# Performance work log

Hardware: AMD Instinct MI355X
Metric: run time of the kernel (lower is better)

Reference implementation:

```python
import jax, jax.numpy as jnp
import numpy as np

TEMP = 0.5
ALPHA, BETA, GAMMA, LAMB = 1e-3, 5e-4, 1e-3, 5e-6
IMG = 1024.0  # img_metas img_shape (H_img, W_img)
LN_EPS = 1e-5


def setup_inputs() -> dict:
    key = jax.random.key(0)
    ks = jax.random.split(key, 20)
    N, C, H, W, NB = 8, 256, 128, 128, 20
    preds_S = jax.random.normal(ks[0], (N, C, H, W), jnp.float32)
    preds_T = jax.random.normal(ks[1], (N, C, H, W), jnp.float32)
    # valid boxes (tl_x, tl_y, br_x, br_y) in pixel coords within [0, IMG]
    raw = jax.random.uniform(ks[2], (N, NB, 4), jnp.float32)
    x1 = raw[..., 0] * 0.7 * IMG
    y1 = raw[..., 1] * 0.7 * IMG
    x2 = jnp.minimum(x1 + (0.05 + raw[..., 2] * 0.25) * IMG, IMG)
    y2 = jnp.minimum(y1 + (0.05 + raw[..., 3] * 0.25) * IMG, IMG)
    gt_bboxes = jnp.stack([x1, y1, x2, y2], axis=-1)
    s = 1.0 / np.sqrt(C)
    s2 = 1.0 / np.sqrt(C // 2)
    mk = lambda k, shape, sc: jax.random.normal(k, shape, jnp.float32) * sc
    return {
        'preds_S': preds_S, 'preds_T': preds_T, 'gt_bboxes': gt_bboxes,
        'w_ms': mk(ks[3], (C,), s), 'b_ms': jnp.zeros((), jnp.float32),
        'w_mt': mk(ks[4], (C,), s), 'b_mt': jnp.zeros((), jnp.float32),
        'w1_s': mk(ks[5], (C // 2, C), s), 'b1_s': jnp.zeros((C // 2,), jnp.float32),
        'g_s': jnp.ones((C // 2,), jnp.float32), 'be_s': jnp.zeros((C // 2,), jnp.float32),
        'w2_s': mk(ks[6], (C, C // 2), s2), 'b2_s': jnp.zeros((C,), jnp.float32),
        'w1_t': mk(ks[7], (C // 2, C), s), 'b1_t': jnp.zeros((C // 2,), jnp.float32),
        'g_t': jnp.ones((C // 2,), jnp.float32), 'be_t': jnp.zeros((C // 2,), jnp.float32),
        'w2_t': mk(ks[8], (C, C // 2), s2), 'b2_t': jnp.zeros((C,), jnp.float32),
    }


def _attention(x):
    # x: [N,C,H,W] -> S_att [N,H,W], C_att [N,C]
    N, C, H, W = x.shape
    v = jnp.abs(x)
    fea = v.mean(axis=1)                                   # [N,H,W]
    S = (H * W) * jax.nn.softmax((fea / TEMP).reshape(N, -1), axis=1)
    ch = v.mean(axis=(2, 3))                               # [N,C]
    Ca = C * jax.nn.softmax(ch / TEMP, axis=1)
    return S.reshape(N, H, W), Ca


def _masks(gt, H, W):
    # gt: [N,nb,4] pixel coords; box-rasterized scatter-max foreground mask
    wmin = jnp.floor(gt[..., 0] / IMG * W)
    wmax = jnp.ceil(gt[..., 2] / IMG * W)
    hmin = jnp.floor(gt[..., 1] / IMG * H)
    hmax = jnp.ceil(gt[..., 3] / IMG * H)
    area = 1.0 / ((hmax + 1.0 - hmin) * (wmax + 1.0 - wmin))  # [N,nb]
    hs = jnp.arange(H, dtype=jnp.float32)[None, None, :, None]
    ws = jnp.arange(W, dtype=jnp.float32)[None, None, None, :]
    inb = (hs >= hmin[:, :, None, None]) & (hs <= hmax[:, :, None, None]) \
        & (ws >= wmin[:, :, None, None]) & (ws <= wmax[:, :, None, None])
    Mask_fg = jnp.where(inb, area[:, :, None, None], 0.0).max(axis=1)  # [N,H,W]
    Mask_bg = jnp.where(Mask_fg > 0, 0.0, 1.0)
    sbg = Mask_bg.sum(axis=(1, 2), keepdims=True)
    Mask_bg = jnp.where(sbg > 0, Mask_bg / sbg, Mask_bg)
    return Mask_fg, Mask_bg


def _spatial_pool(x, w, b):
    N, C, H, W = x.shape
    cm = jnp.einsum('nchw,c->nhw', x, w) + b
    sm = jax.nn.softmax(cm.reshape(N, -1), axis=1).reshape(N, H, W)
    return jnp.einsum('nchw,nhw->nc', x, sm)               # [N,C]


def _channel_add(ctx, w1, b1, g, be, w2, b2):
    y = ctx @ w1.T + b1                                    # [N,C/2]
    m = y.mean(axis=1, keepdims=True)
    v = y.var(axis=1, keepdims=True)
    y = (y - m) / jnp.sqrt(v + LN_EPS) * g + be
    y = jax.nn.relu(y)
    return y @ w2.T + b2                                   # [N,C]


def reference(preds_S, preds_T, gt_bboxes, w_ms, b_ms, w_mt, b_mt,
              w1_s, b1_s, g_s, be_s, w2_s, b2_s,
              w1_t, b1_t, g_t, be_t, w2_t, b2_t):
    N, C, H, W = preds_S.shape
    S_t, C_t = _attention(preds_T)
    S_s, C_s = _attention(preds_S)
    Mask_fg, Mask_bg = _masks(gt_bboxes, H, W)
    # feature losses: (fg_s - fg_t) = (S - T) * sqrt(S_t)*sqrt(C_t)*sqrt(mask)
    wgt = jnp.sqrt(S_t)[:, None] * jnp.sqrt(C_t)[:, :, None, None]
    d = (preds_S - preds_T) * wgt
    fg_loss = jnp.sum((d * jnp.sqrt(Mask_fg)[:, None]) ** 2) / N
    bg_loss = jnp.sum((d * jnp.sqrt(Mask_bg)[:, None]) ** 2) / N
    mask_loss = jnp.sum(jnp.abs(C_s - C_t)) / N + jnp.sum(jnp.abs(S_s - S_t)) / N
    ctx_s = _spatial_pool(preds_S, w_ms, b_ms)
    ctx_t = _spatial_pool(preds_T, w_mt, b_mt)
    add_s = _channel_add(ctx_s, w1_s, b1_s, g_s, be_s, w2_s, b2_s)
    add_t = _channel_add(ctx_t, w1_t, b1_t, g_t, be_t, w2_t, b2_t)
    rd = (preds_S + add_s[:, :, None, None]) - (preds_T + add_t[:, :, None, None])
    rela_loss = jnp.sum(rd ** 2) / N
    return ALPHA * fg_loss + BETA * bg_loss + GAMMA * mask_loss + LAMB * rela_loss
```

## Files before the change

### kernel.cpp

```cpp
#include <hip/hip_runtime.h>
#include <math.h>

#define NN    8
#define CC    256
#define HWHW  16384
#define NBOX  20
#define HALF  131072

constexpr float C_ALPHA = 1e-3f, C_BETA = 5e-4f, C_GAMMA = 1e-3f, C_LAMB = 5e-6f;
constexpr float C_LN_EPS = 1e-5f;

#define OFF_FEA_S   0
#define OFF_FEA_T   262144
#define OFF_CM_S    524288
#define OFF_CM_T    786432
#define OFF_MFG     1048576
#define OFF_PCHS    1179648
#define OFF_PCHT    1310720
#define OFF_PD      1441792
#define OFF_PCTXS   1572864
#define OFF_PCTXT   1703936
#define OFF_CATT    1835008
#define OFF_DSUM    1837056
#define OFF_STATS   1839104
#define OFF_MXP     1839168
#define OFF_ZP      1839680
#define OFF_BG      1840192
#define OFF_SCAL    1840200
#define OFF_Y       1840208
#define OFF_RELAP   1842256

__device__ __forceinline__ float dpp_wave_sum(float x) {
#define DPPADD(ctrl, rm) \
  x += __int_as_float(__builtin_amdgcn_update_dpp(0, __float_as_int(x), ctrl, rm, 0xf, true));
  DPPADD(0x111, 0xf)
  DPPADD(0x112, 0xf)
  DPPADD(0x114, 0xf)
  DPPADD(0x118, 0xf)
  DPPADD(0x142, 0xa)
  DPPADD(0x143, 0xc)
#undef DPPADD
  return x;
}

__device__ __forceinline__ float dpp_wave_max(float x) {
#define DPPMAX(ctrl, rm) { \
  int r_ = __builtin_amdgcn_update_dpp(__float_as_int(x), __float_as_int(x), ctrl, rm, 0xf, false); \
  x = fmaxf(x, __int_as_float(r_)); }
  DPPMAX(0x111, 0xf)
  DPPMAX(0x112, 0xf)
  DPPMAX(0x114, 0xf)
  DPPMAX(0x118, 0xf)
  DPPMAX(0x142, 0xa)
  DPPMAX(0x143, 0xc)
#undef DPPMAX
  return x;
}

__device__ __forceinline__ float block_sum256(float v, float* sm) {
  int tid = threadIdx.x;
  v = dpp_wave_sum(v);
  if ((tid & 63) == 63) sm[tid >> 6] = v;
  __syncthreads();
  float r = sm[0] + sm[1] + sm[2] + sm[3];
  __syncthreads();
  return r;
}

__device__ __forceinline__ float block_max256(float v, float* sm) {
  int tid = threadIdx.x;
  v = dpp_wave_max(v);
  if ((tid & 63) == 63) sm[tid >> 6] = v;
  __syncthreads();
  float r = fmaxf(fmaxf(sm[0], sm[1]), fmaxf(sm[2], sm[3]));
  __syncthreads();
  return r;
}

__global__ __launch_bounds__(512, 2) void k1_pass1(
    const float* __restrict__ S, const float* __restrict__ T,
    const float* __restrict__ w_ms, const float* __restrict__ w_mt,
    float* __restrict__ ws) {
  int tid = threadIdx.x;
  int lane = tid & 63, sl = tid >> 6;
  int pb = blockIdx.x, cs = blockIdx.y, n = blockIdx.z;
  int pix0 = pb * 256 + lane * 4;
  int ch0 = cs * 128 + sl * 16;

  __shared__ float l_wS[128], l_wT[128];
  __shared__ float f_feaS[256], f_feaT[256], f_cmS[256], f_cmT[256];
  __shared__ float l_chS[128], l_chT[128], l_D[128];
  __shared__ float l_sq[8];

  if (tid < 128) {
    l_wS[tid] = w_ms[cs * 128 + tid];
    l_wT[tid] = w_mt[cs * 128 + tid];
  }
  if (tid < 256) {
    f_feaS[tid] = 0.f; f_feaT[tid] = 0.f; f_cmS[tid] = 0.f; f_cmT[tid] = 0.f;
  }
  __syncthreads();

  const float* baseS = S + (size_t)(n * CC + ch0) * HWHW + pix0;
  const float* baseT = T + (size_t)(n * CC + ch0) * HWHW + pix0;

  float fS[4] = {0.f, 0.f, 0.f, 0.f}, fT[4] = {0.f, 0.f, 0.f, 0.f};
  float cS[4] = {0.f, 0.f, 0.f, 0.f}, cT[4] = {0.f, 0.f, 0.f, 0.f};
  float sq = 0.f;

#define PROC1(c, s4, t4, wS_, wT_) { \
    float asx = fabsf(s4.x), asy = fabsf(s4.y), asz = fabsf(s4.z), asw = fabsf(s4.w); \
    float atx = fabsf(t4.x), aty = fabsf(t4.y), atz = fabsf(t4.z), atw = fabsf(t4.w); \
    fS[0] += asx; fS[1] += asy; fS[2] += asz; fS[3] += asw; \
    fT[0] += atx; fT[1] += aty; fT[2] += atz; fT[3] += atw; \
    chS[c] = (asx + asy) + (asz + asw); \
    chT[c] = (atx + aty) + (atz + atw); \
    cS[0] = fmaf(s4.x, wS_, cS[0]); cS[1] = fmaf(s4.y, wS_, cS[1]); \
    cS[2] = fmaf(s4.z, wS_, cS[2]); cS[3] = fmaf(s4.w, wS_, cS[3]); \
    cT[0] = fmaf(t4.x, wT_, cT[0]); cT[1] = fmaf(t4.y, wT_, cT[1]); \
    cT[2] = fmaf(t4.z, wT_, cT[2]); cT[3] = fmaf(t4.w, wT_, cT[3]); \
    float dx = s4.x - t4.x, dy = s4.y - t4.y, dz = s4.z - t4.z, dw = s4.w - t4.w; \
    sq = fmaf(dx, dx, sq); sq = fmaf(dy, dy, sq); \
    sq = fmaf(dz, dz, sq); sq = fmaf(dw, dw, sq); \
    D[c] = (dx + dy) + (dz + dw); }

#pragma unroll 1
  for (int cg = 0; cg < 4; cg++) {
    const float* bS = baseS + (size_t)(cg * 4) * HWHW;
    const float* bT = baseT + (size_t)(cg * 4) * HWHW;
    float4 s0 = *(const float4*)(bS + (size_t)0 * HWHW);
    float4 s1 = *(const float4*)(bS + (size_t)1 * HWHW);
    float4 s2 = *(const float4*)(bS + (size_t)2 * HWHW);
    float4 s3 = *(const float4*)(bS + (size_t)3 * HWHW);
    float4 t0 = *(const float4*)(bT + (size_t)0 * HWHW);
    float4 t1 = *(const float4*)(bT + (size_t)1 * HWHW);
    float4 t2 = *(const float4*)(bT + (size_t)2 * HWHW);
    float4 t3 = *(const float4*)(bT + (size_t)3 * HWHW);
    float wS0 = l_wS[sl * 16 + cg * 4 + 0], wT0 = l_wT[sl * 16 + cg * 4 + 0];
    float wS1 = l_wS[sl * 16 + cg * 4 + 1], wT1 = l_wT[sl * 16 + cg * 4 + 1];
    float wS2 = l_wS[sl * 16 + cg * 4 + 2], wT2 = l_wT[sl * 16 + cg * 4 + 2];
    float wS3 = l_wS[sl * 16 + cg * 4 + 3], wT3 = l_wT[sl * 16 + cg * 4 + 3];
    float chS[4], chT[4], D[4];
    PROC1(0, s0, t0, wS0, wT0)
    PROC1(1, s1, t1, wS1, wT1)
    PROC1(2, s2, t2, wS2, wT2)
    PROC1(3, s3, t3, wS3, wT3)
#pragma unroll
    for (int c = 0; c < 4; c++) {
      float a = dpp_wave_sum(chS[c]);
      float b = dpp_wave_sum(chT[c]);
      float d = dpp_wave_sum(D[c]);
      if (lane == 63) {
        l_chS[sl * 16 + cg * 4 + c] = a;
        l_chT[sl * 16 + cg * 4 + c] = b;
        l_D[sl * 16 + cg * 4 + c]   = d;
      }
    }
  }
#undef PROC1

  atomicAdd(&f_feaS[lane * 4 + 0], fS[0]); atomicAdd(&f_feaS[lane * 4 + 1], fS[1]);
  atomicAdd(&f_feaS[lane * 4 + 2], fS[2]); atomicAdd(&f_feaS[lane * 4 + 3], fS[3]);
  atomicAdd(&f_feaT[lane * 4 + 0], fT[0]); atomicAdd(&f_feaT[lane * 4 + 1], fT[1]);
  atomicAdd(&f_feaT[lane * 4 + 2], fT[2]); atomicAdd(&f_feaT[lane * 4 + 3], fT[3]);
  atomicAdd(&f_cmS[lane * 4 + 0], cS[0]); atomicAdd(&f_cmS[lane * 4 + 1], cS[1]);
  atomicAdd(&f_cmS[lane * 4 + 2], cS[2]); atomicAdd(&f_cmS[lane * 4 + 3], cS[3]);
  atomicAdd(&f_cmT[lane * 4 + 0], cT[0]); atomicAdd(&f_cmT[lane * 4 + 1], cT[1]);
  atomicAdd(&f_cmT[lane * 4 + 2], cT[2]); atomicAdd(&f_cmT[lane * 4 + 3], cT[3]);

  sq = dpp_wave_sum(sq);
  if (lane == 63) l_sq[sl] = sq;
  __syncthreads();

  if (tid < 256) {
    int gp = cs * HALF + n * HWHW + pb * 256 + tid;
    ws[OFF_FEA_S + gp] = f_feaS[tid];
    ws[OFF_FEA_T + gp] = f_feaT[tid];
    ws[OFF_CM_S + gp]  = f_cmS[tid];
    ws[OFF_CM_T + gp]  = f_cmT[tid];
  }
  if (tid < 128) {
    int bo = (n * CC + cs * 128 + tid) * 64 + pb;
    ws[OFF_PCHS + bo] = l_chS[tid];
    ws[OFF_PCHT + bo] = l_chT[tid];
    ws[OFF_PD + bo]   = l_D[tid];
  }
  if (tid == 0) {
    float t = 0.f;
#pragma unroll
    for (int i = 0; i < 8; i++) t += l_sq[i];
    atomicAdd(&ws[OFF_SCAL + 0], t);
  }
}

__global__ __launch_bounds__(256) void k2B_maskstats(const float* __restrict__ gt,
                                                     float* __restrict__ ws) {
  int tid = threadIdx.x;
  int pbB = blockIdx.x, n = blockIdx.y;
  int pix0 = pbB * 1024 + tid * 4;

  __shared__ float bx[NBOX][5];
  __shared__ float l_bg[4];
  __shared__ float sm[4];

  if (tid < NBOX) {
    const float* g = gt + (n * NBOX + tid) * 4;
    float wmin = floorf(g[0] * 0.125f);
    float hmin = floorf(g[1] * 0.125f);
    float wmax = ceilf(g[2] * 0.125f);
    float hmax = ceilf(g[3] * 0.125f);
    bx[tid][0] = wmin; bx[tid][1] = hmin; bx[tid][2] = wmax; bx[tid][3] = hmax;
    bx[tid][4] = 1.0f / ((hmax + 1.0f - hmin) * (wmax + 1.0f - wmin));
  }
  __syncthreads();

  float best[4] = {0.f, 0.f, 0.f, 0.f};
#pragma unroll
  for (int b = 0; b < NBOX; b++) {
    float wmin = bx[b][0], hmin = bx[b][1], wmax = bx[b][2], hmax = bx[b][3];
    float ar = bx[b][4];
#pragma unroll
    for (int j = 0; j < 4; j++) {
      int pix = pix0 + j;
      float hf = (float)(pix >> 7), wf = (float)(pix & 127);
      bool in = (hf >= hmin) && (hf <= hmax) && (wf >= wmin) && (wf <= wmax);
      best[j] = in ? fmaxf(best[j], ar) : best[j];
    }
  }
  float4 bo;
  bo.x = best[0]; bo.y = best[1]; bo.z = best[2]; bo.w = best[3];
  *(float4*)&ws[OFF_MFG + n * HWHW + pix0] = bo;

  float bg = (best[0] > 0.f ? 0.f : 1.f) + (best[1] > 0.f ? 0.f : 1.f) +
             (best[2] > 0.f ? 0.f : 1.f) + (best[3] > 0.f ? 0.f : 1.f);
  bg = dpp_wave_sum(bg);
  if ((tid & 63) == 63) l_bg[tid >> 6] = bg;
  __syncthreads();
  if (tid == 0) atomicAdd(&ws[OFF_BG + n], l_bg[0] + l_bg[1] + l_bg[2] + l_bg[3]);

  int gp = n * HWHW + pix0;
  const int   offs[4]   = {OFF_FEA_S, OFF_FEA_T, OFF_CM_S, OFF_CM_T};
  const float scales[4] = {1.0f / 128.0f, 1.0f / 128.0f, 1.0f, 1.0f};
#pragma unroll
  for (int a = 0; a < 4; a++) {
    float4 v0 = *(const float4*)&ws[offs[a] + gp];
    float4 v1 = *(const float4*)&ws[offs[a] + HALF + gp];
    float sc = scales[a];
    float vx = (v0.x + v1.x) * sc, vy = (v0.y + v1.y) * sc;
    float vz = (v0.z + v1.z) * sc, vw = (v0.w + v1.w) * sc;
    float mx = fmaxf(fmaxf(vx, vy), fmaxf(vz, vw));
    mx = block_max256(mx, sm);
    float z = expf(vx - mx) + expf(vy - mx) + expf(vz - mx) + expf(vw - mx);
    z = block_sum256(z, sm);
    if (tid == 0) {
      ws[OFF_MXP + a * 128 + n * 16 + pbB] = mx;
      ws[OFF_ZP + a * 128 + n * 16 + pbB]  = z;
    }
  }
}

__global__ __launch_bounds__(256) void kC_stats2(float* __restrict__ ws) {
  int tid = threadIdx.x, n = blockIdx.x;
  __shared__ float sm[4];

  float chS = 0.f, chT = 0.f, Dv = 0.f;
  int base = (n * CC + tid) * 64;
#pragma unroll 4
  for (int k = 0; k < 64; k += 4) {
    float4 a = *(const float4*)&ws[OFF_PCHS + base + k];
    float4 b = *(const float4*)&ws[OFF_PCHT + base + k];
    float4 d = *(const float4*)&ws[OFF_PD + base + k];
    chS += (a.x + a.y) + (a.z + a.w);
    chT += (b.x + b.y) + (b.z + b.w);
    Dv  += (d.x + d.y) + (d.z + d.w);
  }
  ws[OFF_DSUM + n * CC + tid] = Dv;

  float lS = chS * (1.0f / 8192.0f), lT = chT * (1.0f / 8192.0f);
  float mS = block_max256(lS, sm);
  float mT = block_max256(lT, sm);
  float eS = expf(lS - mS), eT = expf(lT - mT);
  float ZS = block_sum256(eS, sm);
  float ZT = block_sum256(eT, sm);
  float cattS = (float)CC * eS / ZS;
  float cattT = (float)CC * eT / ZT;
  ws[OFF_CATT + n * CC + tid] = cattT;
  float mml = block_sum256(fabsf(cattS - cattT), sm);
  if (tid == 0) atomicAdd(&ws[OFF_SCAL + 2], mml);

  if (tid < 4) {
    int a = tid;
    float m = -1e30f;
    for (int i = 0; i < 16; i++)
      m = fmaxf(m, ws[OFF_MXP + a * 128 + n * 16 + i]);
    float Z = 0.f;
    for (int i = 0; i < 16; i++)
      Z += ws[OFF_ZP + a * 128 + n * 16 + i] *
           expf(ws[OFF_MXP + a * 128 + n * 16 + i] - m);
    ws[OFF_STATS + n * 8 + 2 * a]     = m;
    ws[OFF_STATS + n * 8 + 2 * a + 1] = Z;
  }
}

__global__ __launch_bounds__(512, 2) void k4_pass2(
    const float* __restrict__ S, const float* __restrict__ T,
    float* __restrict__ ws) {
  int tid = threadIdx.x;
  int lane = tid & 63, sl = tid >> 6;
  int pb = blockIdx.x, cs = blockIdx.y, n = blockIdx.z;
  int pix0 = pb * 256 + lane * 4;
  int ch0 = cs * 128 + sl * 16;

  __shared__ float l_catt[128];
  __shared__ float wcombL[256], smsL[256], smtL[256];
  __shared__ float l_cs[128], l_ct[128], l_c[8];

  if (tid < 128) l_catt[tid] = ws[OFF_CATT + n * CC + cs * 128 + tid];
  if (tid < 64) {
    float mxFS = ws[OFF_STATS + n * 8 + 0], ZFS = ws[OFF_STATS + n * 8 + 1];
    float mxFT = ws[OFF_STATS + n * 8 + 2], ZFT = ws[OFF_STATS + n * 8 + 3];
    float mxCS = ws[OFF_STATS + n * 8 + 4], ZCS = ws[OFF_STATS + n * 8 + 5];
    float mxCT = ws[OFF_STATS + n * 8 + 6], ZCT = ws[OFF_STATS + n * 8 + 7];
    float bgc  = ws[OFF_BG + n];
    int gp = n * HWHW + pb * 256 + tid * 4;
    float4 fS0 = *(const float4*)&ws[OFF_FEA_S + gp];
    float4 fS1 = *(const float4*)&ws[OFF_FEA_S + HALF + gp];
    float4 fT0 = *(const float4*)&ws[OFF_FEA_T + gp];
    float4 fT1 = *(const float4*)&ws[OFF_FEA_T + HALF + gp];
    float4 cS0 = *(const float4*)&ws[OFF_CM_S + gp];
    float4 cS1 = *(const float4*)&ws[OFF_CM_S + HALF + gp];
    float4 cT0 = *(const float4*)&ws[OFF_CM_T + gp];
    float4 cT1 = *(const float4*)&ws[OFF_CM_T + HALF + gp];
    float4 mf = *(const float4*)&ws[OFF_MFG + gp];
    float fSa[4] = {fS0.x + fS1.x, fS0.y + fS1.y, fS0.z + fS1.z, fS0.w + fS1.w};
    float fTa[4] = {fT0.x + fT1.x, fT0.y + fT1.y, fT0.z + fT1.z, fT0.w + fT1.w};
    float cSa[4] = {cS0.x + cS1.x, cS0.y + cS1.y, cS0.z + cS1.z, cS0.w + cS1.w};
    float cTa[4] = {cT0.x + cT1.x, cT0.y + cT1.y, cT0.z + cT1.z, cT0.w + cT1.w};
    float mfa[4] = {mf.x, mf.y, mf.z, mf.w};
    float macc = 0.f;
#pragma unroll
    for (int j = 0; j < 4; j++) {
      float pT = expf(fTa[j] * (1.0f / 128.0f) - mxFT) / ZFT;
      float pS = expf(fSa[j] * (1.0f / 128.0f) - mxFS) / ZFS;
      float Satt = (float)HWHW * pT;
      float mbg = (mfa[j] > 0.f) ? 0.f : ((bgc > 0.f) ? 1.0f / bgc : 1.0f);
      wcombL[tid * 4 + j] = Satt * (C_ALPHA * mfa[j] + C_BETA * mbg);
      smsL[tid * 4 + j] = expf(cSa[j] - mxCS) / ZCS;
      smtL[tid * 4 + j] = expf(cTa[j] - mxCT) / ZCT;
      macc += fabsf(pS - pT);
    }
    macc = dpp_wave_sum(macc);
    if (tid == 63 && cs == 0) atomicAdd(&ws[OFF_SCAL + 2], macc * (float)HWHW);
  }
  __syncthreads();

  float4 sms = *(const float4*)&smsL[lane * 4];
  float4 smt = *(const float4*)&smtL[lane * 4];
  float4 wcb = *(const float4*)&wcombL[lane * 4];

  const float* baseS = S + (size_t)(n * CC + ch0) * HWHW + pix0;
  const float* baseT = T + (size_t)(n * CC + ch0) * HWHW + pix0;

  float aw[4] = {0.f, 0.f, 0.f, 0.f};

#define PROC2(c, s4, t4, ca_) { \
    float dx = s4.x - t4.x, dy = s4.y - t4.y, dz = s4.z - t4.z, dw = s4.w - t4.w; \
    aw[0] = fmaf(dx * dx, ca_, aw[0]); aw[1] = fmaf(dy * dy, ca_, aw[1]); \
    aw[2] = fmaf(dz * dz, ca_, aw[2]); aw[3] = fmaf(dw * dw, ca_, aw[3]); \
    ctxS[c] = fmaf(s4.x, sms.x, fmaf(s4.y, sms.y, fmaf(s4.z, sms.z, s4.w * sms.w))); \
    ctxT[c] = fmaf(t4.x, smt.x, fmaf(t4.y, smt.y, fmaf(t4.z, smt.z, t4.w * smt.w))); }

#pragma unroll 1
  for (int cg = 0; cg < 4; cg++) {
    const float* bS = baseS + (size_t)(cg * 4) * HWHW;
    const float* bT = baseT + (size_t)(cg * 4) * HWHW;
    float4 s0 = *(const float4*)(bS + (size_t)0 * HWHW);
    float4 s1 = *(const float4*)(bS + (size_t)1 * HWHW);
    float4 s2 = *(const float4*)(bS + (size_t)2 * HWHW);
    float4 s3 = *(const float4*)(bS + (size_t)3 * HWHW);
    float4 t0 = *(const float4*)(bT + (size_t)0 * HWHW);
    float4 t1 = *(const float4*)(bT + (size_t)1 * HWHW);
    float4 t2 = *(const float4*)(bT + (size_t)2 * HWHW);
    float4 t3 = *(const float4*)(bT + (size_t)3 * HWHW);
    float ca0 = l_catt[sl * 16 + cg * 4 + 0];
    float ca1 = l_catt[sl * 16 + cg * 4 + 1];
    float ca2 = l_catt[sl * 16 + cg * 4 + 2];
    float ca3 = l_catt[sl * 16 + cg * 4 + 3];
    float ctxS[4], ctxT[4];
    PROC2(0, s0, t0, ca0)
    PROC2(1, s1, t1, ca1)
    PROC2(2, s2, t2, ca2)
    PROC2(3, s3, t3, ca3)
#pragma unroll
    for (int c = 0; c < 4; c++) {
      float xs = dpp_wave_sum(ctxS[c]);
      float xt = dpp_wave_sum(ctxT[c]);
      if (lane == 63) {
        l_cs[sl * 16 + cg * 4 + c] = xs;
        l_ct[sl * 16 + cg * 4 + c] = xt;
      }
    }
  }
#undef PROC2

  float contrib = fmaf(aw[0], wcb.x, fmaf(aw[1], wcb.y, fmaf(aw[2], wcb.z, aw[3] * wcb.w)));
  contrib = dpp_wave_sum(contrib);
  if (lane == 63) l_c[sl] = contrib;
  __syncthreads();

  if (tid < 128) {
    int bo = (n * CC + cs * 128 + tid) * 64 + pb;
    ws[OFF_PCTXS + bo] = l_cs[tid];
    ws[OFF_PCTXT + bo] = l_ct[tid];
  }
  if (tid == 0) {
    float t = 0.f;
#pragma unroll
    for (int i = 0; i < 8; i++) t += l_c[i];
    atomicAdd(&ws[OFF_SCAL + 1], t);
  }
}

__global__ __launch_bounds__(128) void k5a_mlp1(
    const float* __restrict__ w1_s, const float* __restrict__ b1_s,
    const float* __restrict__ g_s,  const float* __restrict__ be_s,
    const float* __restrict__ w1_t, const float* __restrict__ b1_t,
    const float* __restrict__ g_t,  const float* __restrict__ be_t,
    float* __restrict__ ws) {
  int tid = threadIdx.x;
  int n = blockIdx.x >> 1, st = blockIdx.x & 1;
  const float* w1 = st ? w1_t : w1_s;
  const float* b1 = st ? b1_t : b1_s;
  const float* g  = st ? g_t  : g_s;
  const float* be = st ? be_t : be_s;
  int pbase = (st ? OFF_PCTXT : OFF_PCTXS) + n * CC * 64;

  __shared__ float ctx[CC];
  __shared__ float red[2];
#pragma unroll
  for (int half = 0; half < 2; half++) {
    int c = tid + half * 128;
    const float* p = ws + pbase + c * 64;
    float a = 0.f;
#pragma unroll 4
    for (int k = 0; k < 64; k += 4) {
      float4 x = *(const float4*)(p + k);
      a += (x.x + x.y) + (x.z + x.w);
    }
    ctx[c] = a;
  }
  __syncthreads();

  float acc = b1[tid];
  const float* wr = w1 + tid * CC;
#pragma unroll 8
  for (int c = 0; c < CC; c += 4) {
    float4 w = *(const float4*)(wr + c);
    acc = fmaf(w.x, ctx[c], acc);
    acc = fmaf(w.y, ctx[c + 1], acc);
    acc = fmaf(w.z, ctx[c + 2], acc);
    acc = fmaf(w.w, ctx[c + 3], acc);
  }

  float v = dpp_wave_sum(acc);
  if ((tid & 63) == 63) red[tid >> 6] = v;
  __syncthreads();
  float mean = (red[0] + red[1]) * (1.0f / 128.0f);
  __syncthreads();
  float dm = acc - mean;
  v = dpp_wave_sum(dm * dm);
  if ((tid & 63) == 63) red[tid >> 6] = v;
  __syncthreads();
  float var = (red[0] + red[1]) * (1.0f / 128.0f);
  float q = dm * (1.0f / sqrtf(var + C_LN_EPS)) * g[tid] + be[tid];
  ws[OFF_Y + blockIdx.x * 128 + tid] = q > 0.f ? q : 0.f;
}

__global__ __launch_bounds__(256) void k5b_mlp2(
    const float* __restrict__ w2_s, const float* __restrict__ b2_s,
    const float* __restrict__ w2_t, const float* __restrict__ b2_t,
    float* __restrict__ ws) {
  int tid = threadIdx.x, n = blockIdx.x;
  __shared__ float ysh[128], yth[128];
  __shared__ float sm[4];
  if (tid < 128) ysh[tid] = ws[OFF_Y + (n * 2 + 0) * 128 + tid];
  else           yth[tid - 128] = ws[OFF_Y + (n * 2 + 1) * 128 + (tid - 128)];
  __syncthreads();

  float es = b2_s[tid], et = b2_t[tid];
  const float* w2sr = w2_s + tid * 128;
  const float* w2tr = w2_t + tid * 128;
#pragma unroll 8
  for (int j = 0; j < 128; j += 4) {
    float4 a = *(const float4*)(w2sr + j);
    float4 b = *(const float4*)(w2tr + j);
    es = fmaf(a.x, ysh[j], es); es = fmaf(a.y, ysh[j + 1], es);
    es = fmaf(a.z, ysh[j + 2], es); es = fmaf(a.w, ysh[j + 3], es);
    et = fmaf(b.x, yth[j], et); et = fmaf(b.y, yth[j + 1], et);
    et = fmaf(b.z, yth[j + 2], et); et = fmaf(b.w, yth[j + 3], et);
  }
  float e = es - et;
  float rp = 2.0f * e * ws[OFF_DSUM + n * CC + tid] + (float)HWHW * e * e;
  rp = block_sum256(rp, sm);
  if (tid == 0) ws[OFF_RELAP + n] = rp;
}

__global__ __launch_bounds__(64) void k5c_final(float* __restrict__ ws,
                                                float* __restrict__ out) {
  int lane = threadIdx.x;
  float r = (lane < NN) ? ws[OFF_RELAP + lane] : 0.f;
  r = dpp_wave_sum(r);
  if (lane == 63) {
    float rela = ws[OFF_SCAL + 0] + r;
    out[0] = (ws[OFF_SCAL + 1] + C_GAMMA * ws[OFF_SCAL + 2] + C_LAMB * rela) *
             (1.0f / (float)NN);
  }
}

extern "C" void kernel_launch(void* const* d_in, const int* in_sizes, int n_in,
                              void* d_out, int out_size, void* d_ws, size_t ws_size,
                              hipStream_t stream) {
  const float* S    = (const float*)d_in[0];
  const float* T    = (const float*)d_in[1];
  const float* gt   = (const float*)d_in[2];
  const float* w_ms = (const float*)d_in[3];
  const float* w_mt = (const float*)d_in[5];
  const float* w1_s = (const float*)d_in[7];
  const float* b1_s = (const float*)d_in[8];
  const float* g_s  = (const float*)d_in[9];
  const float* be_s = (const float*)d_in[10];
  const float* w2_s = (const float*)d_in[11];
  const float* b2_s = (const float*)d_in[12];
  const float* w1_t = (const float*)d_in[13];
  const float* b1_t = (const float*)d_in[14];
  const float* g_t  = (const float*)d_in[15];
  const float* be_t = (const float*)d_in[16];
  const float* w2_t = (const float*)d_in[17];
  const float* b2_t = (const float*)d_in[18];
  float* ws = (float*)d_ws;
  float* out = (float*)d_out;

  hipMemsetAsync(ws + OFF_BG, 0, 16 * sizeof(float), stream);

  k1_pass1<<<dim3(64, 2, 8), dim3(512), 0, stream>>>(S, T, w_ms, w_mt, ws);
  k2B_maskstats<<<dim3(16, 8), dim3(256), 0, stream>>>(gt, ws);
  kC_stats2<<<dim3(8), dim3(256), 0, stream>>>(ws);
  k4_pass2<<<dim3(64, 2, 8), dim3(512), 0, stream>>>(S, T, ws);
  k5a_mlp1<<<dim3(16), dim3(128), 0, stream>>>(w1_s, b1_s, g_s, be_s,
                                               w1_t, b1_t, g_t, be_t, ws);
  k5b_mlp2<<<dim3(8), dim3(256), 0, stream>>>(w2_s, b2_s, w2_t, b2_t, ws);
  k5c_final<<<dim3(1), dim3(64), 0, stream>>>(ws, out);
}
```

Before: 406.0 us.

## Atomically reduce per-block partials and fuse MLP kernels into one launch

Per-block channel and context partials are now accumulated with global atomicAdd into compact per-(n,c) buffers instead of being written as 64-way partial arrays that later kernels re-read and sum. The two MLP kernels are merged into a single 512-thread kernel per sample, which removes one launch and the intermediate Y round-trip. In exchange there is contention on the atomic adds, a larger memset, and float-atomic summation order becomes nondeterministic.

```diff
diff --git a/kernel.cpp b/kernel.cpp
--- a/kernel.cpp
+++ b/kernel.cpp
@@ -15,20 +15,18 @@
 #define OFF_CM_S    524288
 #define OFF_CM_T    786432
 #define OFF_MFG     1048576
-#define OFF_PCHS    1179648
-#define OFF_PCHT    1310720
-#define OFF_PD      1441792
-#define OFF_PCTXS   1572864
-#define OFF_PCTXT   1703936
-#define OFF_CATT    1835008
-#define OFF_DSUM    1837056
-#define OFF_STATS   1839104
-#define OFF_MXP     1839168
-#define OFF_ZP      1839680
-#define OFF_BG      1840192
-#define OFF_SCAL    1840200
-#define OFF_Y       1840208
-#define OFF_RELAP   1842256
+#define OFF_CHS     1179648
+#define OFF_CHT     1181696
+#define OFF_DSUM    1183744
+#define OFF_CTXS    1185792
+#define OFF_CTXT    1187840
+#define OFF_BG      1189888
+#define OFF_SCAL    1189896
+#define OFF_CATT    1189904
+#define OFF_STATS   1191952
+#define OFF_MXP     1192016
+#define OFF_ZP      1192528
+#define OFF_RELAP   1193040
 
 __device__ __forceinline__ float dpp_wave_sum(float x) {
 #define DPPADD(ctrl, rm) \
@@ -180,10 +178,10 @@
     ws[OFF_CM_T + gp]  = f_cmT[tid];
   }
   if (tid < 128) {
-    int bo = (n * CC + cs * 128 + tid) * 64 + pb;
-    ws[OFF_PCHS + bo] = l_chS[tid];
-    ws[OFF_PCHT + bo] = l_chT[tid];
-    ws[OFF_PD + bo]   = l_D[tid];
+    int co = n * CC + cs * 128 + tid;
+    atomicAdd(&ws[OFF_CHS + co],  l_chS[tid]);
+    atomicAdd(&ws[OFF_CHT + co],  l_chT[tid]);
+    atomicAdd(&ws[OFF_DSUM + co], l_D[tid]);
   }
   if (tid == 0) {
     float t = 0.f;
@@ -263,18 +261,8 @@
   int tid = threadIdx.x, n = blockIdx.x;
   __shared__ float sm[4];
 
-  float chS = 0.f, chT = 0.f, Dv = 0.f;
-  int base = (n * CC + tid) * 64;
-#pragma unroll 4
-  for (int k = 0; k < 64; k += 4) {
-    float4 a = *(const float4*)&ws[OFF_PCHS + base + k];
-    float4 b = *(const float4*)&ws[OFF_PCHT + base + k];
-    float4 d = *(const float4*)&ws[OFF_PD + base + k];
-    chS += (a.x + a.y) + (a.z + a.w);
-    chT += (b.x + b.y) + (b.z + b.w);
-    Dv  += (d.x + d.y) + (d.z + d.w);
-  }
-  ws[OFF_DSUM + n * CC + tid] = Dv;
+  float chS = ws[OFF_CHS + n * CC + tid];
+  float chT = ws[OFF_CHT + n * CC + tid];
 
   float lS = chS * (1.0f / 8192.0f), lT = chT * (1.0f / 8192.0f);
   float mS = block_max256(lS, sm);
@@ -409,9 +397,9 @@
   __syncthreads();
 
   if (tid < 128) {
-    int bo = (n * CC + cs * 128 + tid) * 64 + pb;
-    ws[OFF_PCTXS + bo] = l_cs[tid];
-    ws[OFF_PCTXT + bo] = l_ct[tid];
+    int co = n * CC + cs * 128 + tid;
+    atomicAdd(&ws[OFF_CTXS + co], l_cs[tid]);
+    atomicAdd(&ws[OFF_CTXT + co], l_ct[tid]);
   }
   if (tid == 0) {
     float t = 0.f;
@@ -421,88 +409,90 @@
   }
 }
 
-__global__ __launch_bounds__(128) void k5a_mlp1(
+__global__ __launch_bounds__(512) void k5_mlp(
     const float* __restrict__ w1_s, const float* __restrict__ b1_s,
     const float* __restrict__ g_s,  const float* __restrict__ be_s,
     const float* __restrict__ w1_t, const float* __restrict__ b1_t,
     const float* __restrict__ g_t,  const float* __restrict__ be_t,
-    float* __restrict__ ws) {
-  int tid = threadIdx.x;
-  int n = blockIdx.x >> 1, st = blockIdx.x & 1;
-  const float* w1 = st ? w1_t : w1_s;
-  const float* b1 = st ? b1_t : b1_s;
-  const float* g  = st ? g_t  : g_s;
-  const float* be = st ? be_t : be_s;
-  int pbase = (st ? OFF_PCTXT : OFF_PCTXS) + n * CC * 64;
-
-  __shared__ float ctx[CC];
-  __shared__ float red[2];
-#pragma unroll
-  for (int half = 0; half < 2; half++) {
-    int c = tid + half * 128;
-    const float* p = ws + pbase + c * 64;
-    float a = 0.f;
-#pragma unroll 4
-    for (int k = 0; k < 64; k += 4) {
-      float4 x = *(const float4*)(p + k);
-      a += (x.x + x.y) + (x.z + x.w);
-    }
-    ctx[c] = a;
-  }
-  __syncthreads();
-
-  float acc = b1[tid];
-  const float* wr = w1 + tid * CC;
-#pragma unroll 8
-  for (int c = 0; c < CC; c += 4) {
-    float4 w = *(const float4*)(wr + c);
-    acc = fmaf(w.x, ctx[c], acc);
-    acc = fmaf(w.y, ctx[c + 1], acc);
-    acc = fmaf(w.z, ctx[c + 2], acc);
-    acc = fmaf(w.w, ctx[c + 3], acc);
-  }
-
-  float v = dpp_wave_sum(acc);
-  if ((tid & 63) == 63) red[tid >> 6] = v;
-  __syncthreads();
-  float mean = (red[0] + red[1]) * (1.0f / 128.0f);
-  __syncthreads();
-  float dm = acc - mean;
-  v = dpp_wave_sum(dm * dm);
-  if ((tid & 63) == 63) red[tid >> 6] = v;
-  __syncthreads();
-  float var = (red[0] + red[1]) * (1.0f / 128.0f);
-  float q = dm * (1.0f / sqrtf(var + C_LN_EPS)) * g[tid] + be[tid];
-  ws[OFF_Y + blockIdx.x * 128 + tid] = q > 0.f ? q : 0.f;
-}
-
-__global__ __launch_bounds__(256) void k5b_mlp2(
     const float* __restrict__ w2_s, const float* __restrict__ b2_s,
     const float* __restrict__ w2_t, const float* __restrict__ b2_t,
     float* __restrict__ ws) {
   int tid = threadIdx.x, n = blockIdx.x;
-  __shared__ float ysh[128], yth[128];
-  __shared__ float sm[4];
-  if (tid < 128) ysh[tid] = ws[OFF_Y + (n * 2 + 0) * 128 + tid];
-  else           yth[tid - 128] = ws[OFF_Y + (n * 2 + 1) * 128 + (tid - 128)];
-  __syncthreads();
-
-  float es = b2_s[tid], et = b2_t[tid];
-  const float* w2sr = w2_s + tid * 128;
-  const float* w2tr = w2_t + tid * 128;
+  int lane = tid & 63;
+  __shared__ float ctxS[CC], ctxT[CC], ysh[128], yth[128];
+  __shared__ float red[4], smr[8];
+
+  if (tid < 256)      ctxS[tid] = ws[OFF_CTXS + n * CC + tid];
+  else                ctxT[tid - 256] = ws[OFF_CTXT + n * CC + (tid - 256)];
+  __syncthreads();
+
+  int st = (tid >> 7) & 1, j = tid & 127;
+  float acc = 0.f;
+  if (tid < 256) {
+    const float* w1 = st ? w1_t : w1_s;
+    const float* b1 = st ? b1_t : b1_s;
+    const float* ctx = st ? ctxT : ctxS;
+    acc = b1[j];
+    const float* wr = w1 + j * CC;
 #pragma unroll 8
-  for (int j = 0; j < 128; j += 4) {
-    float4 a = *(const float4*)(w2sr + j);
-    float4 b = *(const float4*)(w2tr + j);
-    es = fmaf(a.x, ysh[j], es); es = fmaf(a.y, ysh[j + 1], es);
-    es = fmaf(a.z, ysh[j + 2], es); es = fmaf(a.w, ysh[j + 3], es);
-    et = fmaf(b.x, yth[j], et); et = fmaf(b.y, yth[j + 1], et);
-    et = fmaf(b.z, yth[j + 2], et); et = fmaf(b.w, yth[j + 3], et);
-  }
-  float e = es - et;
-  float rp = 2.0f * e * ws[OFF_DSUM + n * CC + tid] + (float)HWHW * e * e;
-  rp = block_sum256(rp, sm);
-  if (tid == 0) ws[OFF_RELAP + n] = rp;
+    for (int c = 0; c < CC; c += 4) {
+      float4 w = *(const float4*)(wr + c);
+      acc = fmaf(w.x, ctx[c], acc);
+      acc = fmaf(w.y, ctx[c + 1], acc);
+      acc = fmaf(w.z, ctx[c + 2], acc);
+      acc = fmaf(w.w, ctx[c + 3], acc);
+    }
+  }
+
+  float v = dpp_wave_sum(acc);
+  if (tid < 256 && lane == 63) red[tid >> 6] = v;
+  __syncthreads();
+  int grp = tid >> 7;
+  float mean = 0.f;
+  if (tid < 256) mean = (red[grp * 2] + red[grp * 2 + 1]) * (1.0f / 128.0f);
+  __syncthreads();
+  float dm = acc - mean;
+  v = dpp_wave_sum(dm * dm);
+  if (tid < 256 && lane == 63) red[tid >> 6] = v;
+  __syncthreads();
+  if (tid < 256) {
+    float var = (red[grp * 2] + red[grp * 2 + 1]) * (1.0f / 128.0f);
+    const float* g  = st ? g_t  : g_s;
+    const float* be = st ? be_t : be_s;
+    float q = dm * (1.0f / sqrtf(var + C_LN_EPS)) * g[j] + be[j];
+    q = q > 0.f ? q : 0.f;
+    if (st == 0) ysh[j] = q;
+    else         yth[j] = q;
+  }
+  __syncthreads();
+
+  float rp = 0.f;
+  if (tid < 256) {
+    int c = tid;
+    float es = b2_s[c], et = b2_t[c];
+    const float* w2sr = w2_s + c * 128;
+    const float* w2tr = w2_t + c * 128;
+#pragma unroll 8
+    for (int jj = 0; jj < 128; jj += 4) {
+      float4 a = *(const float4*)(w2sr + jj);
+      float4 b = *(const float4*)(w2tr + jj);
+      es = fmaf(a.x, ysh[jj], es); es = fmaf(a.y, ysh[jj + 1], es);
+      es = fmaf(a.z, ysh[jj + 2], es); es = fmaf(a.w, ysh[jj + 3], es);
+      et = fmaf(b.x, yth[jj], et); et = fmaf(b.y, yth[jj + 1], et);
+      et = fmaf(b.z, yth[jj + 2], et); et = fmaf(b.w, yth[jj + 3], et);
+    }
+    float e = es - et;
+    rp = 2.0f * e * ws[OFF_DSUM + n * CC + c] + (float)HWHW * e * e;
+  }
+  rp = dpp_wave_sum(rp);
+  if (lane == 63) smr[tid >> 6] = rp;
+  __syncthreads();
+  if (tid == 0) {
+    float t = 0.f;
+#pragma unroll
+    for (int i = 0; i < 8; i++) t += smr[i];
+    ws[OFF_RELAP + n] = t;
+  }
 }
 
 __global__ __launch_bounds__(64) void k5c_final(float* __restrict__ ws,
@@ -540,14 +530,14 @@
   float* ws = (float*)d_ws;
   float* out = (float*)d_out;
 
-  hipMemsetAsync(ws + OFF_BG, 0, 16 * sizeof(float), stream);
+  hipMemsetAsync(ws + OFF_CHS, 0, 10256 * sizeof(float), stream);
 
   k1_pass1<<<dim3(64, 2, 8), dim3(512), 0, stream>>>(S, T, w_ms, w_mt, ws);
   k2B_maskstats<<<dim3(16, 8), dim3(256), 0, stream>>>(gt, ws);
   kC_stats2<<<dim3(8), dim3(256), 0, stream>>>(ws);
   k4_pass2<<<dim3(64, 2, 8), dim3(512), 0, stream>>>(S, T, ws);
-  k5a_mlp1<<<dim3(16), dim3(128), 0, stream>>>(w1_s, b1_s, g_s, be_s,
-                                               w1_t, b1_t, g_t, be_t, ws);
-  k5b_mlp2<<<dim3(8), dim3(256), 0, stream>>>(w2_s, b2_s, w2_t, b2_t, ws);
+  k5_mlp<<<dim3(8), dim3(512), 0, stream>>>(w1_s, b1_s, g_s, be_s,
+                                            w1_t, b1_t, g_t, be_t,
+                                            w2_s, b2_s, w2_t, b2_t, ws);
   k5c_final<<<dim3(1), dim3(64), 0, stream>>>(ws, out);
 }
```

Measured after the change: 398.8 us. Within noise of the previous version (-1.8%).
